# Performance work log

Hardware: AMD Instinct MI355X
Metric: run time of the kernel (lower is better)

The kernel has to match this reference:

```python
import jax, jax.numpy as jnp
import numpy as np

T, D, F, E, K = 2048, 1024, 4096, 8, 2


def setup_inputs() -> dict:
    key = jax.random.key(0)
    ks = jax.random.split(key, 4)
    return {
        "x": jax.random.normal(ks[0], (T, D), dtype=jnp.float32),
        "Wg": jax.random.normal(ks[1], (D, E), dtype=jnp.float32) * (1.0 / np.sqrt(D)),
        "bg": jnp.zeros((E,), dtype=jnp.float32),
        "W1": jax.random.normal(ks[2], (E, D, F), dtype=jnp.float32) * (1.0 / np.sqrt(D)),
        "b1": jnp.zeros((E, F), dtype=jnp.float32),
        "W2": jax.random.normal(ks[3], (E, F, D), dtype=jnp.float32) * (1.0 / np.sqrt(F)),
        "b2": jnp.zeros((E, D), dtype=jnp.float32),
        "top_k": K,
    }


def reference(x, Wg, bg, W1, b1, W2, b2, top_k):
    num_tokens, d_model = x.shape
    n_experts = W1.shape[0]

    # Gate + baseline top-k routing: router returns top-k softmax probs.
    gate_logits = x @ Wg + bg                       # [T, E]
    gate_probs_all = jax.nn.softmax(gate_logits, axis=-1)
    top_k_probs, top_k_indices = jax.lax.top_k(gate_probs_all, top_k)  # [T, K]

    # Load-balancing aux loss (top-1 token counts x mean gate prob).
    top1 = top_k_indices[:, 0]
    tokens_per_expert = jnp.zeros((n_experts,), x.dtype).at[top1].add(1.0)
    aux_loss = jnp.sum(tokens_per_expert / (num_tokens + 1e-8)
                       * gate_probs_all.mean(axis=0)) * n_experts

    # Combine weights: scatter top-k probs into dense [T, E]; zero elsewhere,
    # so the dense per-expert compute below reproduces the sparse dispatch math.
    comb = jnp.zeros((num_tokens, n_experts), x.dtype)
    comb = comb.at[jnp.arange(num_tokens)[:, None], top_k_indices].add(top_k_probs)

    # Expert FFNs (linear_fc1 -> relu -> linear_fc2), batched over experts.
    h = jax.nn.relu(jnp.einsum('td,edf->etf', x, W1) + b1[:, None, :])  # [E, T, F]
    y = jnp.einsum('etf,efd->etd', h, W2) + b2[:, None, :]              # [E, T, D]

    # Weighted scatter-combine.
    output = jnp.einsum('etd,te->td', y, comb)                          # [T, D]
    return output, aux_loss
```

## Files before the change

### kernel.cpp

```cpp
#include <hip/hip_runtime.h>
#include <stdint.h>

#define T_TOK 2048
#define DMODEL 1024
#define FDIM 4096
#define NEXP 8
#define CAP 2048

typedef __attribute__((ext_vector_type(8))) short short8;
typedef __attribute__((ext_vector_type(4))) float f32x4;
typedef __attribute__((ext_vector_type(4))) unsigned short us4;
typedef __attribute__((ext_vector_type(8))) unsigned short us8;

__device__ __forceinline__ unsigned short f2bf(float f) {
  union { float f; unsigned int u; } v; v.f = f;
  unsigned int r = (v.u + 0x7fffu + ((v.u >> 16) & 1u)) >> 16;
  return (unsigned short)r;
}

__device__ __forceinline__ void async16(const unsigned short* g, unsigned short* l) {
  __builtin_amdgcn_global_load_lds(
      (const __attribute__((address_space(1))) unsigned int*)g,
      (__attribute__((address_space(3))) unsigned int*)l,
      16, 0, 0);
}

__device__ __forceinline__ void stage64(const unsigned short* Ar0, const unsigned short* Ar1,
                                        const unsigned short* Br0, const unsigned short* Br1,
                                        int ko, unsigned short* Ab, unsigned short* Bb) {
  async16(Ar0 + ko,     Ab);
  async16(Ar1 + ko,     Ab + 512);
  async16(Ar0 + ko + 8, Ab + 1024);
  async16(Ar1 + ko + 8, Ab + 1536);
  async16(Br0 + ko,     Bb);
  async16(Br1 + ko,     Bb + 512);
  async16(Br0 + ko + 8, Bb + 1024);
  async16(Br1 + ko + 8, Bb + 1536);
}

__global__ void gate_kernel(const float* __restrict__ x, const float* __restrict__ Wg,
                            const float* __restrict__ bg,
                            int* cnt, int* top1cnt, float* sumprob,
                            int* list, float* wlist, int* tok2slot) {
  int wave = threadIdx.x >> 6;
  int lane = threadIdx.x & 63;
  __shared__ float sprob[8];
  __shared__ int   stop1[8];
  __shared__ int   ent_e[32];
  __shared__ float ent_p[32];
  if (threadIdx.x < 8) { sprob[threadIdx.x] = 0.f; stop1[threadIdx.x] = 0; }
  __syncthreads();

#pragma unroll
  for (int i = 0; i < 4; i++) {
    int s = wave * 4 + i;
    int t = blockIdx.x * 16 + s;
    float acc[8];
#pragma unroll
    for (int e = 0; e < 8; e++) acc[e] = 0.f;
    const float* xr = x + (size_t)t * DMODEL;
    for (int c = lane; c < DMODEL / 4; c += 64) {
      f32x4 xv = ((const f32x4*)xr)[c];
      const float* wr = Wg + (size_t)c * 4 * 8;
#pragma unroll
      for (int q = 0; q < 4; q++)
#pragma unroll
        for (int e = 0; e < 8; e++) acc[e] += xv[q] * wr[q * 8 + e];
    }
#pragma unroll
    for (int off = 32; off > 0; off >>= 1) {
#pragma unroll
      for (int e = 0; e < 8; e++) acc[e] += __shfl_down(acc[e], off);
    }
    if (lane == 0) {
      float p[8];
      float m = -1e30f;
#pragma unroll
      for (int e = 0; e < 8; e++) { p[e] = acc[e] + bg[e]; m = fmaxf(m, p[e]); }
      float sum = 0.f;
#pragma unroll
      for (int e = 0; e < 8; e++) { p[e] = __expf(p[e] - m); sum += p[e]; }
      float inv = 1.f / sum;
#pragma unroll
      for (int e = 0; e < 8; e++) p[e] *= inv;
      int e1 = 0; float p1 = p[0];
#pragma unroll
      for (int e = 1; e < 8; e++) if (p[e] > p1) { p1 = p[e]; e1 = e; }
      int e2 = -1; float p2 = -1.f;
#pragma unroll
      for (int e = 0; e < 8; e++) if (e != e1 && p[e] > p2) { p2 = p[e]; e2 = e; }
      atomicAdd(&stop1[e1], 1);
#pragma unroll
      for (int e = 0; e < 8; e++) atomicAdd(&sprob[e], p[e]);
      ent_e[2 * s]     = e1; ent_p[2 * s]     = p1;
      ent_e[2 * s + 1] = e2; ent_p[2 * s + 1] = p2;
    }
  }
  __syncthreads();

  if (threadIdx.x < 8) {
    int e = threadIdx.x;
    int n = 0;
#pragma unroll
    for (int j = 0; j < 32; j++) n += (ent_e[j] == e) ? 1 : 0;
    if (n) {
      int pos = atomicAdd(cnt + e, n);
#pragma unroll
      for (int j = 0; j < 32; j++) {
        if (ent_e[j] == e) {
          int t = blockIdx.x * 16 + (j >> 1);
          list[e * CAP + pos]  = t;
          wlist[e * CAP + pos] = ent_p[j];
          tok2slot[2 * t + (j & 1)] = (e << 16) | pos;
          pos++;
        }
      }
    }
    atomicAdd(sumprob + e, sprob[e]);
    int c = stop1[e];
    if (c) atomicAdd(top1cnt + e, c);
  }
}

__global__ void offs_aux_kernel(const int* cnt, const int* top1cnt, const float* sumprob,
                                int* offs, float* out_aux) {
  if (threadIdx.x == 0 && blockIdx.x == 0) {
    int off = 0;
    float aux = 0.f;
    for (int e = 0; e < 8; e++) {
      offs[e] = off; off += cnt[e];
      aux += ((float)top1cnt[e] / ((float)T_TOK + 1e-8f)) * (sumprob[e] / (float)T_TOK);
    }
    *out_aux = aux * (float)NEXP;
  }
}

__global__ void gather_kernel(const float* __restrict__ x, const int* __restrict__ list,
                              const int* __restrict__ cnt, const int* __restrict__ offs,
                              unsigned short* __restrict__ xg) {
  int e = blockIdx.x >> 11;
  int i = blockIdx.x & 2047;
  if (i >= cnt[e]) return;
  int t = list[e * CAP + i];
  int row = offs[e] + i;
  const f32x4* src = (const f32x4*)(x + (size_t)t * DMODEL);
  us4* dst = (us4*)(xg + (size_t)row * DMODEL);
  int j = threadIdx.x;
  f32x4 v = src[j];
  us4 o; o.x = f2bf(v.x); o.y = f2bf(v.y); o.z = f2bf(v.z); o.w = f2bf(v.w);
  dst[j] = o;
}

__launch_bounds__(256)
__global__ void convt_kernel(const float* __restrict__ in, unsigned short* __restrict__ out,
                             int Kfull, int Nfull, int KS, int k_off, int NS, int n_off) {
  int e = blockIdx.y;
  int ntn = NS >> 6;
  int tk = blockIdx.x / ntn, tn = blockIdx.x % ntn;
  const float* src = in + (size_t)e * Kfull * Nfull + (size_t)(k_off + tk * 64) * Nfull + n_off + tn * 64;
  unsigned short* dst = out + (size_t)e * NS * KS + (size_t)(tn * 64) * KS + tk * 64;
  __shared__ unsigned short Ls[64 * 72];
  int t = threadIdx.x;
  int k = t >> 4, n4 = (t & 15) * 4;
#pragma unroll
  for (int i = 0; i < 4; i++) {
    int kk = k + 16 * i;
    f32x4 v = *(const f32x4*)&src[(size_t)kk * Nfull + n4];
    Ls[(n4 + 0) * 72 + kk] = f2bf(v.x);
    Ls[(n4 + 1) * 72 + kk] = f2bf(v.y);
    Ls[(n4 + 2) * 72 + kk] = f2bf(v.z);
    Ls[(n4 + 3) * 72 + kk] = f2bf(v.w);
  }
  __syncthreads();
  int n = t >> 3, k8 = (t & 7) * 8;
#pragma unroll
  for (int j = 0; j < 2; j++) {
    int nn = n + 32 * j;
    us8 v = *(const us8*)&Ls[nn * 72 + k8];
    *(us8*)&dst[(size_t)nn * KS + k8] = v;
  }
}

__launch_bounds__(256)
__global__ void gemm1_kernel(const unsigned short* __restrict__ xg,
                             const unsigned short* __restrict__ Wt,
                             const float* __restrict__ b1,
                             const int* __restrict__ cnt, const int* __restrict__ offs,
                             unsigned short* __restrict__ h, int NS, int n_off) {
  int e = blockIdx.x;
  int mt = blockIdx.z;
  int count = cnt[e];
  if (mt * 128 >= count) return;
  int nloc = blockIdx.y * 128;
  int base = offs[e];
  const unsigned short* A = xg + (size_t)(base + mt * 128) * DMODEL;
  const unsigned short* B = Wt + (size_t)e * NS * DMODEL + (size_t)nloc * DMODEL;

  __shared__ unsigned short As[2 * 8 * 128 * 8];
  __shared__ unsigned short Bs[2 * 8 * 128 * 8];

  int tid = threadIdx.x;
  int w = tid >> 6, lane = tid & 63;
  int wr = w >> 1, wc = w & 1;
  int l16 = lane & 15, quad = lane >> 4;

  f32x4 acc[4][4];
#pragma unroll
  for (int i = 0; i < 4; i++)
#pragma unroll
    for (int j = 0; j < 4; j++)
#pragma unroll
      for (int r = 0; r < 4; r++) acc[i][j][r] = 0.f;

  const unsigned short* Ar0 = A + (size_t)lane * DMODEL + w * 16;
  const unsigned short* Ar1 = A + (size_t)(64 + lane) * DMODEL + w * 16;
  const unsigned short* Br0 = B + (size_t)lane * DMODEL + w * 16;
  const unsigned short* Br1 = B + (size_t)(64 + lane) * DMODEL + w * 16;

  stage64(Ar0, Ar1, Br0, Br1, 0, &As[w * 2048], &Bs[w * 2048]);
  __syncthreads();

  int cb = 0;
  const int KT = DMODEL / 64;
  for (int kt = 0; kt < KT; kt++) {
    if (kt + 1 < KT)
      stage64(Ar0, Ar1, Br0, Br1, (kt + 1) * 64,
              &As[(cb ^ 1) * 8192 + w * 2048], &Bs[(cb ^ 1) * 8192 + w * 2048]);
    const unsigned short* Ac = &As[cb * 8192 + quad * 1024];
    const unsigned short* Bc = &Bs[cb * 8192 + quad * 1024];
    short8 a0[4], a1[4], b0[4], b1v[4];
#pragma unroll
    for (int i = 0; i < 4; i++) {
      a0[i]  = *(const short8*)&Ac[(wr * 64 + i * 16 + l16) * 8];
      a1[i]  = *(const short8*)&Ac[4096 + (wr * 64 + i * 16 + l16) * 8];
    }
#pragma unroll
    for (int j = 0; j < 4; j++) {
      b0[j]  = *(const short8*)&Bc[(wc * 64 + j * 16 + l16) * 8];
      b1v[j] = *(const short8*)&Bc[4096 + (wc * 64 + j * 16 + l16) * 8];
    }
#pragma unroll
    for (int i = 0; i < 4; i++)
#pragma unroll
      for (int j = 0; j < 4; j++)
        acc[i][j] = __builtin_amdgcn_mfma_f32_16x16x32_bf16(a0[i], b0[j], acc[i][j], 0, 0, 0);
#pragma unroll
    for (int i = 0; i < 4; i++)
#pragma unroll
      for (int j = 0; j < 4; j++)
        acc[i][j] = __builtin_amdgcn_mfma_f32_16x16x32_bf16(a1[i], b1v[j], acc[i][j], 0, 0, 0);
    __syncthreads();
    cb ^= 1;
  }

#pragma unroll
  for (int j = 0; j < 4; j++) {
    int ncl = nloc + wc * 64 + j * 16 + l16;
    float bias = b1[e * FDIM + n_off + ncl];
#pragma unroll
    for (int i = 0; i < 4; i++) {
      int rbase = mt * 128 + wr * 64 + i * 16 + quad * 4;
#pragma unroll
      for (int r = 0; r < 4; r++) {
        int row = rbase + r;
        if (row < count) {
          float v = fmaxf(acc[i][j][r] + bias, 0.f);
          h[(size_t)(base + row) * NS + ncl] = f2bf(v);
        }
      }
    }
  }
}

__launch_bounds__(256)
__global__ void gemm2_kernel(const unsigned short* __restrict__ h,
                             const unsigned short* __restrict__ Wt,
                             const float* __restrict__ b2,
                             const int* __restrict__ cnt, const int* __restrict__ offs,
                             float* __restrict__ y, int KS, int first) {
  int e = blockIdx.x;
  int mt = blockIdx.z;
  int count = cnt[e];
  if (mt * 128 >= count) return;
  int nloc = blockIdx.y * 128;
  int base = offs[e];
  const unsigned short* A = h + (size_t)(base + mt * 128) * KS;
  const unsigned short* B = Wt + (size_t)e * DMODEL * KS + (size_t)nloc * KS;

  __shared__ unsigned short As[2 * 8 * 128 * 8];
  __shared__ unsigned short Bs[2 * 8 * 128 * 8];

  int tid = threadIdx.x;
  int w = tid >> 6, lane = tid & 63;
  int wr = w >> 1, wc = w & 1;
  int l16 = lane & 15, quad = lane >> 4;

  f32x4 acc[4][4];
#pragma unroll
  for (int i = 0; i < 4; i++)
#pragma unroll
    for (int j = 0; j < 4; j++)
#pragma unroll
      for (int r = 0; r < 4; r++) acc[i][j][r] = 0.f;

  const unsigned short* Ar0 = A + (size_t)lane * KS + w * 16;
  const unsigned short* Ar1 = A + (size_t)(64 + lane) * KS + w * 16;
  const unsigned short* Br0 = B + (size_t)lane * KS + w * 16;
  const unsigned short* Br1 = B + (size_t)(64 + lane) * KS + w * 16;

  stage64(Ar0, Ar1, Br0, Br1, 0, &As[w * 2048], &Bs[w * 2048]);
  __syncthreads();

  int cb = 0;
  const int KT = KS / 64;
  for (int kt = 0; kt < KT; kt++) {
    if (kt + 1 < KT)
      stage64(Ar0, Ar1, Br0, Br1, (kt + 1) * 64,
              &As[(cb ^ 1) * 8192 + w * 2048], &Bs[(cb ^ 1) * 8192 + w * 2048]);
    const unsigned short* Ac = &As[cb * 8192 + quad * 1024];
    const unsigned short* Bc = &Bs[cb * 8192 + quad * 1024];
    short8 a0[4], a1[4], b0[4], b1v[4];
#pragma unroll
    for (int i = 0; i < 4; i++) {
      a0[i]  = *(const short8*)&Ac[(wr * 64 + i * 16 + l16) * 8];
      a1[i]  = *(const short8*)&Ac[4096 + (wr * 64 + i * 16 + l16) * 8];
    }
#pragma unroll
    for (int j = 0; j < 4; j++) {
      b0[j]  = *(const short8*)&Bc[(wc * 64 + j * 16 + l16) * 8];
      b1v[j] = *(const short8*)&Bc[4096 + (wc * 64 + j * 16 + l16) * 8];
    }
#pragma unroll
    for (int i = 0; i < 4; i++)
#pragma unroll
      for (int j = 0; j < 4; j++)
        acc[i][j] = __builtin_amdgcn_mfma_f32_16x16x32_bf16(a0[i], b0[j], acc[i][j], 0, 0, 0);
#pragma unroll
    for (int i = 0; i < 4; i++)
#pragma unroll
      for (int j = 0; j < 4; j++)
        acc[i][j] = __builtin_amdgcn_mfma_f32_16x16x32_bf16(a1[i], b1v[j], acc[i][j], 0, 0, 0);
    __syncthreads();
    cb ^= 1;
  }

  float bv[4];
#pragma unroll
  for (int j = 0; j < 4; j++)
    bv[j] = first ? b2[e * DMODEL + nloc + wc * 64 + j * 16 + l16] : 0.f;

#pragma unroll
  for (int i = 0; i < 4; i++) {
    int rbase = mt * 128 + wr * 64 + i * 16 + quad * 4;
#pragma unroll
    for (int r = 0; r < 4; r++) {
      int row = rbase + r;
      if (row >= count) continue;
      float* yr = y + (size_t)(base + row) * DMODEL;
#pragma unroll
      for (int j = 0; j < 4; j++) {
        int ncol = nloc + wc * 64 + j * 16 + l16;
        float v = acc[i][j][r] + bv[j];
        if (first) yr[ncol] = v;
        else       yr[ncol] += v;
      }
    }
  }
}

__global__ void combine_kernel(const float* __restrict__ y, const int* __restrict__ offs,
                               const int* __restrict__ tok2slot, const float* __restrict__ wlist,
                               float* __restrict__ out) {
  int t = blockIdx.x;
  int s0 = tok2slot[2 * t], s1 = tok2slot[2 * t + 1];
  int e0 = s0 >> 16, p0 = s0 & 0xffff;
  int e1 = s1 >> 16, p1 = s1 & 0xffff;
  float w0 = wlist[e0 * CAP + p0], w1 = wlist[e1 * CAP + p1];
  int r0 = offs[e0] + p0, r1 = offs[e1] + p1;
  int j = threadIdx.x * 4;
  f32x4 a = *(const f32x4*)&y[(size_t)r0 * DMODEL + j];
  f32x4 b = *(const f32x4*)&y[(size_t)r1 * DMODEL + j];
  f32x4 o;
  o.x = w0 * a.x + w1 * b.x;
  o.y = w0 * a.y + w1 * b.y;
  o.z = w0 * a.z + w1 * b.z;
  o.w = w0 * a.w + w1 * b.w;
  *(f32x4*)&out[(size_t)t * DMODEL + j] = o;
}

extern "C" void kernel_launch(void* const* d_in, const int* in_sizes, int n_in,
                              void* d_out, int out_size, void* d_ws, size_t ws_size,
                              hipStream_t stream) {
  const float* x  = (const float*)d_in[0];
  const float* Wg = (const float*)d_in[1];
  const float* bg = (const float*)d_in[2];
  const float* W1 = (const float*)d_in[3];
  const float* b1 = (const float*)d_in[4];
  const float* W2 = (const float*)d_in[5];
  const float* b2 = (const float*)d_in[6];
  float* out = (float*)d_out;

  char* ws = (char*)d_ws;
  int*   cnt      = (int*)(ws + 0);
  int*   top1cnt  = (int*)(ws + 32);
  int*   offs     = (int*)(ws + 64);
  float* sumprob  = (float*)(ws + 96);
  int*   list     = (int*)(ws + 4096);
  float* wlist    = (float*)(ws + 69632);
  int*   tok2slot = (int*)(ws + 135168);
  unsigned short* xg = (unsigned short*)(ws + 151552);

  const size_t fixed = 8540160ull + 16777216ull;
  int S = 8;
  if      (ws_size >= fixed + 100663296ull)     S = 1;
  else if (ws_size >= fixed + 100663296ull / 2) S = 2;
  else if (ws_size >= fixed + 100663296ull / 4) S = 4;
  const int NS1 = FDIM / S;
  unsigned short* h  = (unsigned short*)(ws + 8540160);
  float*          y  = (float*)(ws + 8540160 + 33554432ull / S);
  unsigned short* Wt = (unsigned short*)(ws + 8540160 + 33554432ull / S + 16777216ull);

  hipMemsetAsync(ws, 0, 1024, stream);

  gate_kernel<<<T_TOK / 16, 256, 0, stream>>>(x, Wg, bg, cnt, top1cnt, sumprob, list, wlist, tok2slot);
  offs_aux_kernel<<<1, 64, 0, stream>>>(cnt, top1cnt, sumprob, offs, out + (size_t)T_TOK * DMODEL);
  gather_kernel<<<NEXP * CAP, 256, 0, stream>>>(x, list, cnt, offs, xg);

  for (int s = 0; s < S; s++) {
    convt_kernel<<<dim3((DMODEL / 64) * (NS1 / 64), NEXP), 256, 0, stream>>>(
        W1, Wt, DMODEL, FDIM, DMODEL, 0, NS1, s * NS1);
    gemm1_kernel<<<dim3(NEXP, NS1 / 128, 16), 256, 0, stream>>>(
        xg, Wt, b1, cnt, offs, h, NS1, s * NS1);
    convt_kernel<<<dim3((NS1 / 64) * (DMODEL / 64), NEXP), 256, 0, stream>>>(
        W2, Wt, FDIM, DMODEL, NS1, s * NS1, DMODEL, 0);
    gemm2_kernel<<<dim3(NEXP, DMODEL / 128, 16), 256, 0, stream>>>(
        h, Wt, b2, cnt, offs, y, NS1, s == 0 ? 1 : 0);
  }

  combine_kernel<<<T_TOK, 256, 0, stream>>>(y, offs, tok2slot, wlist, out);
}
```

Baseline: 607.2 us.

## Triple-buffer LDS staging with explicit vmcnt waits in both expert GEMMs

Both expert GEMM kernels move from a double-buffered LDS pipeline to a three-stage one that prefetches two K-tiles ahead. Partial s_waitcnt vmcnt counts replace the full __syncthreads, so loads for later tiles stay in flight while the current tile is consumed. A second barrier after the LDS fragment reads keeps the buffer being refilled from being overwritten too early. This hides more global-load latency behind the MFMA work, at the cost of more LDS per block, which may lower occupancy, and hand-counted vmcnt values that depend on stage64 issuing exactly 8 loads.

```diff
diff --git a/kernel.cpp b/kernel.cpp
--- a/kernel.cpp
+++ b/kernel.cpp
@@ -196,8 +196,8 @@
   const unsigned short* A = xg + (size_t)(base + mt * 128) * DMODEL;
   const unsigned short* B = Wt + (size_t)e * NS * DMODEL + (size_t)nloc * DMODEL;
 
-  __shared__ unsigned short As[2 * 8 * 128 * 8];
-  __shared__ unsigned short Bs[2 * 8 * 128 * 8];
+  __shared__ unsigned short As[3 * 8 * 128 * 8];
+  __shared__ unsigned short Bs[3 * 8 * 128 * 8];
 
   int tid = threadIdx.x;
   int w = tid >> 6, lane = tid & 63;
@@ -217,17 +217,26 @@
   const unsigned short* Br0 = B + (size_t)lane * DMODEL + w * 16;
   const unsigned short* Br1 = B + (size_t)(64 + lane) * DMODEL + w * 16;
 
-  stage64(Ar0, Ar1, Br0, Br1, 0, &As[w * 2048], &Bs[w * 2048]);
-  __syncthreads();
-
-  int cb = 0;
+  stage64(Ar0, Ar1, Br0, Br1, 0,  &As[0 * 8192 + w * 2048], &Bs[0 * 8192 + w * 2048]);
+  stage64(Ar0, Ar1, Br0, Br1, 64, &As[1 * 8192 + w * 2048], &Bs[1 * 8192 + w * 2048]);
+
   const int KT = DMODEL / 64;
   for (int kt = 0; kt < KT; kt++) {
-    if (kt + 1 < KT)
-      stage64(Ar0, Ar1, Br0, Br1, (kt + 1) * 64,
-              &As[(cb ^ 1) * 8192 + w * 2048], &Bs[(cb ^ 1) * 8192 + w * 2048]);
-    const unsigned short* Ac = &As[cb * 8192 + quad * 1024];
-    const unsigned short* Bc = &Bs[cb * 8192 + quad * 1024];
+    int buf = kt % 3;
+    if (kt + 2 < KT) {
+      int nb = (kt + 2) % 3;
+      stage64(Ar0, Ar1, Br0, Br1, (kt + 2) * 64,
+              &As[nb * 8192 + w * 2048], &Bs[nb * 8192 + w * 2048]);
+      asm volatile("s_waitcnt vmcnt(16)" ::: "memory");
+    } else if (kt + 1 < KT) {
+      asm volatile("s_waitcnt vmcnt(8)" ::: "memory");
+    } else {
+      asm volatile("s_waitcnt vmcnt(0)" ::: "memory");
+    }
+    __builtin_amdgcn_s_barrier();
+    __builtin_amdgcn_sched_barrier(0);
+    const unsigned short* Ac = &As[buf * 8192 + quad * 1024];
+    const unsigned short* Bc = &Bs[buf * 8192 + quad * 1024];
     short8 a0[4], a1[4], b0[4], b1v[4];
 #pragma unroll
     for (int i = 0; i < 4; i++) {
@@ -239,6 +248,9 @@
       b0[j]  = *(const short8*)&Bc[(wc * 64 + j * 16 + l16) * 8];
       b1v[j] = *(const short8*)&Bc[4096 + (wc * 64 + j * 16 + l16) * 8];
     }
+    asm volatile("s_waitcnt lgkmcnt(0)" ::: "memory");
+    __builtin_amdgcn_sched_barrier(0);
+    __builtin_amdgcn_s_barrier();
 #pragma unroll
     for (int i = 0; i < 4; i++)
 #pragma unroll
@@ -249,8 +261,6 @@
 #pragma unroll
       for (int j = 0; j < 4; j++)
         acc[i][j] = __builtin_amdgcn_mfma_f32_16x16x32_bf16(a1[i], b1v[j], acc[i][j], 0, 0, 0);
-    __syncthreads();
-    cb ^= 1;
   }
 
 #pragma unroll
@@ -287,8 +297,8 @@
   const unsigned short* A = h + (size_t)(base + mt * 128) * KS;
   const unsigned short* B = Wt + (size_t)e * DMODEL * KS + (size_t)nloc * KS;
 
-  __shared__ unsigned short As[2 * 8 * 128 * 8];
-  __shared__ unsigned short Bs[2 * 8 * 128 * 8];
+  __shared__ unsigned short As[3 * 8 * 128 * 8];
+  __shared__ unsigned short Bs[3 * 8 * 128 * 8];
 
   int tid = threadIdx.x;
   int w = tid >> 6, lane = tid & 63;
@@ -308,17 +318,26 @@
   const unsigned short* Br0 = B + (size_t)lane * KS + w * 16;
   const unsigned short* Br1 = B + (size_t)(64 + lane) * KS + w * 16;
 
-  stage64(Ar0, Ar1, Br0, Br1, 0, &As[w * 2048], &Bs[w * 2048]);
-  __syncthreads();
-
-  int cb = 0;
+  stage64(Ar0, Ar1, Br0, Br1, 0,  &As[0 * 8192 + w * 2048], &Bs[0 * 8192 + w * 2048]);
+  stage64(Ar0, Ar1, Br0, Br1, 64, &As[1 * 8192 + w * 2048], &Bs[1 * 8192 + w * 2048]);
+
   const int KT = KS / 64;
   for (int kt = 0; kt < KT; kt++) {
-    if (kt + 1 < KT)
-      stage64(Ar0, Ar1, Br0, Br1, (kt + 1) * 64,
-              &As[(cb ^ 1) * 8192 + w * 2048], &Bs[(cb ^ 1) * 8192 + w * 2048]);
-    const unsigned short* Ac = &As[cb * 8192 + quad * 1024];
-    const unsigned short* Bc = &Bs[cb * 8192 + quad * 1024];
+    int buf = kt % 3;
+    if (kt + 2 < KT) {
+      int nb = (kt + 2) % 3;
+      stage64(Ar0, Ar1, Br0, Br1, (kt + 2) * 64,
+              &As[nb * 8192 + w * 2048], &Bs[nb * 8192 + w * 2048]);
+      asm volatile("s_waitcnt vmcnt(16)" ::: "memory");
+    } else if (kt + 1 < KT) {
+      asm volatile("s_waitcnt vmcnt(8)" ::: "memory");
+    } else {
+      asm volatile("s_waitcnt vmcnt(0)" ::: "memory");
+    }
+    __builtin_amdgcn_s_barrier();
+    __builtin_amdgcn_sched_barrier(0);
+    const unsigned short* Ac = &As[buf * 8192 + quad * 1024];
+    const unsigned short* Bc = &Bs[buf * 8192 + quad * 1024];
     short8 a0[4], a1[4], b0[4], b1v[4];
 #pragma unroll
     for (int i = 0; i < 4; i++) {
@@ -330,6 +349,9 @@
       b0[j]  = *(const short8*)&Bc[(wc * 64 + j * 16 + l16) * 8];
       b1v[j] = *(const short8*)&Bc[4096 + (wc * 64 + j * 16 + l16) * 8];
     }
+    asm volatile("s_waitcnt lgkmcnt(0)" ::: "memory");
+    __builtin_amdgcn_sched_barrier(0);
+    __builtin_amdgcn_s_barrier();
 #pragma unroll
     for (int i = 0; i < 4; i++)
 #pragma unroll
@@ -340,8 +362,6 @@
 #pragma unroll
       for (int j = 0; j < 4; j++)
         acc[i][j] = __builtin_amdgcn_mfma_f32_16x16x32_bf16(a1[i], b1v[j], acc[i][j], 0, 0, 0);
-    __syncthreads();
-    cb ^= 1;
   }
 
   float bv[4];
```

Measured after the change: 706.9 us. 1.16x slower.
